# Optimization experiments

Hardware: AMD Instinct MI355X
Metric: run time of the kernel (lower is better)

Reference implementation:

```python
import jax, jax.numpy as jnp
import numpy as np

B, S, D_IN, D_H, D_ACT = 16, 2048, 1024, 2048, 1024


def setup_inputs() -> dict:
    key = jax.random.key(0)
    ks = jax.random.split(key, 8)
    s_in = 1.0 / np.sqrt(D_IN)
    s_h = 1.0 / np.sqrt(D_H)
    return {
        "x": jax.random.normal(ks[0], (B, S, D_IN), dtype=jnp.float32),
        "W_init": jax.random.uniform(ks[1], (D_H, D_IN), jnp.float32, -s_in, s_in),
        "b_init": jax.random.uniform(ks[2], (D_H,), jnp.float32, -s_in, s_in),
        "W_ih": jax.random.uniform(ks[3], (D_H, D_H), jnp.float32, -s_h, s_h),
        "b_ih": jax.random.uniform(ks[4], (D_H,), jnp.float32, -s_h, s_h),
        "b_hh": jax.random.uniform(ks[5], (D_H,), jnp.float32, -s_h, s_h),
        "W_final": jax.random.uniform(ks[6], (D_ACT, D_H), jnp.float32, -s_h, s_h),
        "b_final": jax.random.uniform(ks[7], (D_ACT,), jnp.float32, -s_h, s_h),
    }


def reference(x, W_init, b_init, W_ih, b_ih, b_hh, W_final, b_final):
    # initial linear + relu: [B,S,D_IN] -> [B,S,D_H]
    h = jax.nn.relu(jnp.einsum('bsi,hi->bsh', x, W_init) + b_init)
    # per-timestep RNN with hidden reset to zero each step: the W_hh term
    # vanishes, so each step is relu(W_ih @ h_t + b_ih + b_hh) -> one GEMM.
    out = jax.nn.relu(jnp.einsum('bsh,gh->bsg', h, W_ih) + b_ih + b_hh)
    # final linear: [B,S,D_H] -> [B,S,D_ACT]
    return jnp.einsum('bsh,ah->bsa', out, W_final) + b_final
```

## Files before the change

kernel.cpp:

```cpp
#include <hip/hip_runtime.h>
#include <hip/hip_bf16.h>
#include <stdint.h>
#include <stddef.h>

typedef __bf16 bf16;
typedef __bf16 bf16x8 __attribute__((ext_vector_type(8)));
typedef float f32x4 __attribute__((ext_vector_type(4)));
typedef __attribute__((address_space(1))) void gvoid;
typedef __attribute__((address_space(3))) void lvoid;

#define FENCE() asm volatile("" ::: "memory")
#define VMCNT(n) asm volatile("s_waitcnt vmcnt(" #n ")" ::: "memory")
#define BARS() do { FENCE(); __builtin_amdgcn_s_barrier(); FENCE(); } while (0)

__global__ __launch_bounds__(256)
void cvt_f32_bf16(const float* __restrict__ in, bf16* __restrict__ out, int n8)
{
    int i = blockIdx.x * 256 + threadIdx.x;
    if (i >= n8) return;
    const f32x4* p = (const f32x4*)in + (size_t)i * 2;
    f32x4 a = p[0], b = p[1];
    bf16x8 o;
    o[0] = (bf16)a[0]; o[1] = (bf16)a[1]; o[2] = (bf16)a[2]; o[3] = (bf16)a[3];
    o[4] = (bf16)b[0]; o[5] = (bf16)b[1]; o[6] = (bf16)b[2]; o[7] = (bf16)b[3];
    *((bf16x8*)out + i) = o;
}

#define RDA(buf, mh) \
    _Pragma("unroll") \
    for (int m_ = 0; m_ < 4; ++m_) { \
        af[m_][0] = *(const bf16x8*)(rdA0 + (buf) * 16384 + ((mh) + m_) * 1024); \
        af[m_][1] = *(const bf16x8*)(rdA1 + (buf) * 16384 + ((mh) + m_) * 1024); \
    }

#define RDB(buf, dst, nb) \
    _Pragma("unroll") \
    for (int n_ = 0; n_ < 2; ++n_) { \
        dst[n_][0] = *(const bf16x8*)(rdB0 + (buf) * 16384 + ((nb) + n_) * 1024); \
        dst[n_][1] = *(const bf16x8*)(rdB1 + (buf) * 16384 + ((nb) + n_) * 1024); \
    }

#define STAGE(gsrc, lreg, h, kt) do { \
        const bf16* g_ = (gsrc) + (size_t)((h) * 128) * K + (size_t)(kt) * 64; \
        bf16* l_ = (lreg) + (h) * 8192 + wave * 1024; \
        __builtin_amdgcn_global_load_lds((gvoid*)g_,           (lvoid*)l_,         16, 0, 0); \
        __builtin_amdgcn_global_load_lds((gvoid*)(g_ + rowK8), (lvoid*)(l_ + 512), 16, 0, 0); \
    } while (0)

#define QUAD(mh, nh, bb) \
    _Pragma("unroll") \
    for (int h_ = 0; h_ < 2; ++h_) \
        _Pragma("unroll") \
        for (int m_ = 0; m_ < 4; ++m_) \
            _Pragma("unroll") \
            for (int n_ = 0; n_ < 2; ++n_) \
                acc[(mh)+m_][(nh)+n_] = __builtin_amdgcn_mfma_f32_16x16x32_bf16( \
                    af[m_][h_], bb[n_][h_], acc[(mh)+m_][(nh)+n_], 0, 0, 0);

#define MFMA_PH(mh, nh, bb) do { \
        __builtin_amdgcn_s_setprio(1); QUAD(mh, nh, bb); __builtin_amdgcn_s_setprio(0); \
    } while (0)

template<int RELU, int TWO_BIAS, int OUTF32>
__global__ __launch_bounds__(512, 2)
void gemm256(const bf16* __restrict__ A, const bf16* __restrict__ Bm,
             const float* __restrict__ bias1, const float* __restrict__ bias2,
             void* __restrict__ Cp, int M, int N, int K)
{
    extern __shared__ bf16 smem[];
    bf16* As = smem;
    bf16* Bs = smem + 32768;

    const int tid  = threadIdx.x;
    const int wave = tid >> 6;
    const int lane = tid & 63;
    const int wr   = wave >> 2;
    const int wc   = wave & 3;

    const int nwg = gridDim.x * gridDim.y;
    int wg = blockIdx.y * gridDim.x + blockIdx.x;
    wg = (wg & 7) * (nwg >> 3) + (wg >> 3);
    const int bn = wg % gridDim.x;
    const int bm = wg / gridDim.x;

    const int rc  = lane >> 3;
    const int sgc = ((lane & 7) ^ rc) * 8;
    const bf16* aS0 = A  + (size_t)(bm * 256 + wave * 16 + rc) * K + sgc;
    const bf16* bS0 = Bm + (size_t)(bn * 256 + wave * 16 + rc) * K + sgc;
    const size_t rowK8 = (size_t)8 * K;

    const int frow = lane & 15;
    const int fg   = lane >> 4;
    const int fsw  = frow & 7;

    const bf16* rdA0 = As + wr * 8192 + frow * 64 + ((fg ^ fsw) << 3);
    const bf16* rdA1 = As + wr * 8192 + frow * 64 + (((fg + 4) ^ fsw) << 3);
    const bf16* rdB0 = Bs + (wc >> 1) * 8192 + (wc & 1) * 4096 + frow * 64 + ((fg ^ fsw) << 3);
    const bf16* rdB1 = Bs + (wc >> 1) * 8192 + (wc & 1) * 4096 + frow * 64 + (((fg + 4) ^ fsw) << 3);

    bf16x8 af[4][2], bl[2][2], bh[2][2];
    f32x4 acc[8][4];
    #pragma unroll
    for (int i = 0; i < 8; ++i)
        #pragma unroll
        for (int j = 0; j < 4; ++j)
            acc[i][j] = {0.f, 0.f, 0.f, 0.f};

    const int NT = K >> 6;
    const int NI = NT >> 1;

    STAGE(bS0, Bs,         0, 0); STAGE(bS0, Bs,         1, 0);
    STAGE(aS0, As,         0, 0); STAGE(aS0, As,         1, 0);
    STAGE(bS0, Bs + 16384, 0, 1); STAGE(bS0, Bs + 16384, 1, 1);
    VMCNT(4);
    BARS();

    for (int it = 0; it < NI; ++it) {
        const int t1 = 2 * it + 1;
        const int t2 = (2 * it + 2 < NT) ? 2 * it + 2 : 0;
        const int t3 = t2 + 1;

        RDB(0, bl, 0);
        RDA(0, 0);
        STAGE(aS0, As + 16384, 0, t1);
        BARS();
        MFMA_PH(0, 0, bl);
        RDB(0, bh, 2);
        STAGE(aS0, As + 16384, 1, t1);
        BARS();
        MFMA_PH(0, 2, bh);
        RDA(0, 4);
        BARS();
        MFMA_PH(4, 0, bl);
        STAGE(bS0, Bs, 0, t2);
        STAGE(bS0, Bs, 1, t2);
        VMCNT(4);
        BARS();
        MFMA_PH(4, 2, bh);
        RDB(1, bl, 0);
        RDA(1, 0);
        STAGE(aS0, As, 0, t2);
        BARS();
        MFMA_PH(0, 0, bl);
        RDB(1, bh, 2);
        STAGE(aS0, As, 1, t2);
        BARS();
        MFMA_PH(0, 2, bh);
        RDA(1, 4);
        BARS();
        MFMA_PH(4, 0, bl);
        STAGE(bS0, Bs + 16384, 0, t3);
        STAGE(bS0, Bs + 16384, 1, t3);
        VMCNT(4);
        BARS();
        MFMA_PH(4, 2, bh);
    }
    VMCNT(0);

    const int crow0 = bm * 256 + wr * 128 + (lane >> 4) * 4;
    const int ccol0 = bn * 256 + wc * 64 + (lane & 15);

    float bv[4];
    #pragma unroll
    for (int n = 0; n < 4; ++n) {
        bv[n] = bias1[ccol0 + n * 16];
        if (TWO_BIAS) bv[n] += bias2[ccol0 + n * 16];
    }

    #pragma unroll
    for (int m = 0; m < 8; ++m) {
        #pragma unroll
        for (int r = 0; r < 4; ++r) {
            const size_t row = (size_t)(crow0 + m * 16 + r);
            #pragma unroll
            for (int n = 0; n < 4; ++n) {
                float v = acc[m][n][r] + bv[n];
                if (RELU) v = fmaxf(v, 0.0f);
                if (OUTF32)
                    ((float*)Cp)[row * N + ccol0 + n * 16] = v;
                else
                    ((bf16*)Cp)[row * N + ccol0 + n * 16] = (bf16)v;
            }
        }
    }
}

static inline int cvt_blocks(size_t n) { return (int)((n / 8 + 255) / 256); }

extern "C" void kernel_launch(void* const* d_in, const int* in_sizes, int n_in,
                              void* d_out, int out_size, void* d_ws, size_t ws_size,
                              hipStream_t stream) {
    const float* x       = (const float*)d_in[0];
    const float* W_init  = (const float*)d_in[1];
    const float* b_init  = (const float*)d_in[2];
    const float* W_ih    = (const float*)d_in[3];
    const float* b_ih    = (const float*)d_in[4];
    const float* b_hh    = (const float*)d_in[5];
    const float* W_final = (const float*)d_in[6];
    const float* b_final = (const float*)d_in[7];
    float* out = (float*)d_out;

    const int D_H   = in_sizes[2];
    const int D_IN  = in_sizes[1] / D_H;
    const int D_ACT = in_sizes[7];
    const int M     = in_sizes[0] / D_IN;

    const size_t nx  = (size_t)M * D_IN;
    const size_t nw1 = (size_t)D_H * D_IN;
    const size_t nw2 = (size_t)D_H * D_H;
    const size_t nw3 = (size_t)D_ACT * D_H;
    const size_t nh  = (size_t)M * D_H;

    char* ws  = (char*)d_ws;
    bf16* h   = (bf16*)ws;
    bf16* a2  = (bf16*)(ws + nh * 2);
    bf16* xb  = a2;
    bf16* w1b = (bf16*)(ws + nh * 4);
    bf16* w2b = w1b + nw1;
    bf16* w3b = w2b + nw2;

    (void)hipFuncSetAttribute(reinterpret_cast<const void*>(&gemm256<1, 0, 0>),
                              hipFuncAttributeMaxDynamicSharedMemorySize, 131072);
    (void)hipFuncSetAttribute(reinterpret_cast<const void*>(&gemm256<1, 1, 0>),
                              hipFuncAttributeMaxDynamicSharedMemorySize, 131072);
    (void)hipFuncSetAttribute(reinterpret_cast<const void*>(&gemm256<0, 0, 1>),
                              hipFuncAttributeMaxDynamicSharedMemorySize, 131072);

    cvt_f32_bf16<<<cvt_blocks(nx),  256, 0, stream>>>(x,       xb,  (int)(nx  / 8));
    cvt_f32_bf16<<<cvt_blocks(nw1), 256, 0, stream>>>(W_init,  w1b, (int)(nw1 / 8));
    cvt_f32_bf16<<<cvt_blocks(nw2), 256, 0, stream>>>(W_ih,    w2b, (int)(nw2 / 8));
    cvt_f32_bf16<<<cvt_blocks(nw3), 256, 0, stream>>>(W_final, w3b, (int)(nw3 / 8));

    gemm256<1, 0, 0><<<dim3(D_H / 256, M / 256), 512, 131072, stream>>>(
        xb, w1b, b_init, nullptr, h, M, D_H, D_IN);

    gemm256<1, 1, 0><<<dim3(D_H / 256, M / 256), 512, 131072, stream>>>(
        h, w2b, b_ih, b_hh, a2, M, D_H, D_H);

    gemm256<0, 0, 1><<<dim3(D_ACT / 256, M / 256), 512, 131072, stream>>>(
        a2, w3b, b_final, nullptr, out, M, D_ACT, D_H);
}
```

Baseline: 699.8 us.

## Switch GEMM to 32x32x16 MFMA with restructured LDS read and prefetch schedule

Replaces the 16x16x32 bf16 MFMA tiling with 32x32x16 MFMA, so each wave holds 4x2 accumulators of 16 floats, and rewrites the LDS fragment addressing to match. The main loop is rescheduled into eight k-substeps with even/odd register double-buffering of fragments, and A and B tiles are staged together with full vmcnt(0) waits. The goal is fewer LDS reads per FLOP and denser MFMA issue. The cost is that the stricter vmcnt(0) waits may expose more global-load latency than the old partial waits did.

```diff
diff --git a/kernel.cpp b/kernel.cpp
--- a/kernel.cpp
+++ b/kernel.cpp
@@ -6,6 +6,7 @@
 typedef __bf16 bf16;
 typedef __bf16 bf16x8 __attribute__((ext_vector_type(8)));
 typedef float f32x4 __attribute__((ext_vector_type(4)));
+typedef float f32x16 __attribute__((ext_vector_type(16)));
 typedef __attribute__((address_space(1))) void gvoid;
 typedef __attribute__((address_space(3))) void lvoid;
 
@@ -26,19 +27,14 @@
     *((bf16x8*)out + i) = o;
 }
 
-#define RDA(buf, mh) \
-    _Pragma("unroll") \
-    for (int m_ = 0; m_ < 4; ++m_) { \
-        af[m_][0] = *(const bf16x8*)(rdA0 + (buf) * 16384 + ((mh) + m_) * 1024); \
-        af[m_][1] = *(const bf16x8*)(rdA1 + (buf) * 16384 + ((mh) + m_) * 1024); \
-    }
-
-#define RDB(buf, dst, nb) \
-    _Pragma("unroll") \
-    for (int n_ = 0; n_ < 2; ++n_) { \
-        dst[n_][0] = *(const bf16x8*)(rdB0 + (buf) * 16384 + ((nb) + n_) * 1024); \
-        dst[n_][1] = *(const bf16x8*)(rdB1 + (buf) * 16384 + ((nb) + n_) * 1024); \
-    }
+#define RD6(aset, bset, buf, ks) do { \
+        aset[0] = *(const bf16x8*)(aAddr[ks] + (buf) * 16384 + 0 * 2048); \
+        aset[1] = *(const bf16x8*)(aAddr[ks] + (buf) * 16384 + 1 * 2048); \
+        aset[2] = *(const bf16x8*)(aAddr[ks] + (buf) * 16384 + 2 * 2048); \
+        aset[3] = *(const bf16x8*)(aAddr[ks] + (buf) * 16384 + 3 * 2048); \
+        bset[0] = *(const bf16x8*)(bAddr[ks] + (buf) * 16384 + 0 * 2048); \
+        bset[1] = *(const bf16x8*)(bAddr[ks] + (buf) * 16384 + 1 * 2048); \
+    } while (0)
 
 #define STAGE(gsrc, lreg, h, kt) do { \
         const bf16* g_ = (gsrc) + (size_t)((h) * 128) * K + (size_t)(kt) * 64; \
@@ -47,18 +43,15 @@
         __builtin_amdgcn_global_load_lds((gvoid*)(g_ + rowK8), (lvoid*)(l_ + 512), 16, 0, 0); \
     } while (0)
 
-#define QUAD(mh, nh, bb) \
-    _Pragma("unroll") \
-    for (int h_ = 0; h_ < 2; ++h_) \
+#define MFMA8(aset, bset) do { \
+        __builtin_amdgcn_s_setprio(1); \
         _Pragma("unroll") \
-        for (int m_ = 0; m_ < 4; ++m_) \
+        for (int mb_ = 0; mb_ < 4; ++mb_) \
             _Pragma("unroll") \
-            for (int n_ = 0; n_ < 2; ++n_) \
-                acc[(mh)+m_][(nh)+n_] = __builtin_amdgcn_mfma_f32_16x16x32_bf16( \
-                    af[m_][h_], bb[n_][h_], acc[(mh)+m_][(nh)+n_], 0, 0, 0);
-
-#define MFMA_PH(mh, nh, bb) do { \
-        __builtin_amdgcn_s_setprio(1); QUAD(mh, nh, bb); __builtin_amdgcn_s_setprio(0); \
+            for (int nb_ = 0; nb_ < 2; ++nb_) \
+                acc[mb_][nb_] = __builtin_amdgcn_mfma_f32_32x32x16_bf16( \
+                    aset[mb_], bset[nb_], acc[mb_][nb_], 0, 0, 0); \
+        __builtin_amdgcn_s_setprio(0); \
     } while (0)
 
 template<int RELU, int TWO_BIAS, int OUTF32>
@@ -89,97 +82,103 @@
     const bf16* bS0 = Bm + (size_t)(bn * 256 + wave * 16 + rc) * K + sgc;
     const size_t rowK8 = (size_t)8 * K;
 
-    const int frow = lane & 15;
-    const int fg   = lane >> 4;
-    const int fsw  = frow & 7;
-
-    const bf16* rdA0 = As + wr * 8192 + frow * 64 + ((fg ^ fsw) << 3);
-    const bf16* rdA1 = As + wr * 8192 + frow * 64 + (((fg + 4) ^ fsw) << 3);
-    const bf16* rdB0 = Bs + (wc >> 1) * 8192 + (wc & 1) * 4096 + frow * 64 + ((fg ^ fsw) << 3);
-    const bf16* rdB1 = Bs + (wc >> 1) * 8192 + (wc & 1) * 4096 + frow * 64 + (((fg + 4) ^ fsw) << 3);
-
-    bf16x8 af[4][2], bl[2][2], bh[2][2];
-    f32x4 acc[8][4];
-    #pragma unroll
-    for (int i = 0; i < 8; ++i)
+    const int l31 = lane & 31;
+    const int lh  = lane >> 5;
+    const int fsw = lane & 7;
+
+    const bf16* aAddr[4];
+    const bf16* bAddr[4];
+    #pragma unroll
+    for (int ks = 0; ks < 4; ++ks) {
+        const int slot = (2 * ks + lh) ^ fsw;
+        aAddr[ks] = As + wr * 8192 + l31 * 64 + slot * 8;
+        bAddr[ks] = Bs + (wc >> 1) * 8192 + (wc & 1) * 4096 + l31 * 64 + slot * 8;
+    }
+
+    bf16x8 afE[4], afO[4], bbE[2], bbO[2];
+    f32x16 acc[4][2];
+    #pragma unroll
+    for (int i = 0; i < 4; ++i)
         #pragma unroll
-        for (int j = 0; j < 4; ++j)
-            acc[i][j] = {0.f, 0.f, 0.f, 0.f};
+        for (int j = 0; j < 2; ++j)
+            acc[i][j] = (f32x16)(0.f);
 
     const int NT = K >> 6;
     const int NI = NT >> 1;
 
-    STAGE(bS0, Bs,         0, 0); STAGE(bS0, Bs,         1, 0);
-    STAGE(aS0, As,         0, 0); STAGE(aS0, As,         1, 0);
-    STAGE(bS0, Bs + 16384, 0, 1); STAGE(bS0, Bs + 16384, 1, 1);
-    VMCNT(4);
+    STAGE(aS0, As, 0, 0); STAGE(aS0, As, 1, 0);
+    STAGE(bS0, Bs, 0, 0); STAGE(bS0, Bs, 1, 0);
+    VMCNT(0);
     BARS();
+    RD6(afE, bbE, 0, 0);
 
     for (int it = 0; it < NI; ++it) {
         const int t1 = 2 * it + 1;
         const int t2 = (2 * it + 2 < NT) ? 2 * it + 2 : 0;
-        const int t3 = t2 + 1;
-
-        RDB(0, bl, 0);
-        RDA(0, 0);
+
+        BARS();
+        MFMA8(afE, bbE);
+        RD6(afO, bbO, 0, 1);
         STAGE(aS0, As + 16384, 0, t1);
-        BARS();
-        MFMA_PH(0, 0, bl);
-        RDB(0, bh, 2);
         STAGE(aS0, As + 16384, 1, t1);
         BARS();
-        MFMA_PH(0, 2, bh);
-        RDA(0, 4);
-        BARS();
-        MFMA_PH(4, 0, bl);
+        MFMA8(afO, bbO);
+        RD6(afE, bbE, 0, 2);
+        STAGE(bS0, Bs + 16384, 0, t1);
+        STAGE(bS0, Bs + 16384, 1, t1);
+        BARS();
+        MFMA8(afE, bbE);
+        RD6(afO, bbO, 0, 3);
+        VMCNT(0);
+        BARS();
+        MFMA8(afO, bbO);
+        RD6(afE, bbE, 1, 0);
+        BARS();
+        MFMA8(afE, bbE);
+        RD6(afO, bbO, 1, 1);
+        STAGE(aS0, As, 0, t2);
+        STAGE(aS0, As, 1, t2);
+        BARS();
+        MFMA8(afO, bbO);
+        RD6(afE, bbE, 1, 2);
         STAGE(bS0, Bs, 0, t2);
         STAGE(bS0, Bs, 1, t2);
-        VMCNT(4);
-        BARS();
-        MFMA_PH(4, 2, bh);
-        RDB(1, bl, 0);
-        RDA(1, 0);
-        STAGE(aS0, As, 0, t2);
-        BARS();
-        MFMA_PH(0, 0, bl);
-        RDB(1, bh, 2);
-        STAGE(aS0, As, 1, t2);
-        BARS();
-        MFMA_PH(0, 2, bh);
-        RDA(1, 4);
-        BARS();
-        MFMA_PH(4, 0, bl);
-        STAGE(bS0, Bs + 16384, 0, t3);
-        STAGE(bS0, Bs + 16384, 1, t3);
-        VMCNT(4);
-        BARS();
-        MFMA_PH(4, 2, bh);
+        BARS();
+        MFMA8(afE, bbE);
+        RD6(afO, bbO, 1, 3);
+        VMCNT(0);
+        BARS();
+        MFMA8(afO, bbO);
+        RD6(afE, bbE, 0, 0);
     }
     VMCNT(0);
 
-    const int crow0 = bm * 256 + wr * 128 + (lane >> 4) * 4;
-    const int ccol0 = bn * 256 + wc * 64 + (lane & 15);
-
-    float bv[4];
-    #pragma unroll
-    for (int n = 0; n < 4; ++n) {
-        bv[n] = bias1[ccol0 + n * 16];
-        if (TWO_BIAS) bv[n] += bias2[ccol0 + n * 16];
-    }
-
-    #pragma unroll
-    for (int m = 0; m < 8; ++m) {
+    const int crow0 = bm * 256 + wr * 128 + 4 * lh;
+    const int ccol0 = bn * 256 + wc * 64 + l31;
+
+    float bv[2];
+    #pragma unroll
+    for (int nb = 0; nb < 2; ++nb) {
+        bv[nb] = bias1[ccol0 + nb * 32];
+        if (TWO_BIAS) bv[nb] += bias2[ccol0 + nb * 32];
+    }
+
+    #pragma unroll
+    for (int mb = 0; mb < 4; ++mb) {
         #pragma unroll
-        for (int r = 0; r < 4; ++r) {
-            const size_t row = (size_t)(crow0 + m * 16 + r);
+        for (int rq = 0; rq < 4; ++rq) {
             #pragma unroll
-            for (int n = 0; n < 4; ++n) {
-                float v = acc[m][n][r] + bv[n];
-                if (RELU) v = fmaxf(v, 0.0f);
-                if (OUTF32)
-                    ((float*)Cp)[row * N + ccol0 + n * 16] = v;
-                else
-                    ((bf16*)Cp)[row * N + ccol0 + n * 16] = (bf16)v;
+            for (int rl = 0; rl < 4; ++rl) {
+                const size_t row = (size_t)(crow0 + mb * 32 + rq * 8 + rl);
+                #pragma unroll
+                for (int nb = 0; nb < 2; ++nb) {
+                    float v = acc[mb][nb][rq * 4 + rl] + bv[nb];
+                    if (RELU) v = fmaxf(v, 0.0f);
+                    if (OUTF32)
+                        ((float*)Cp)[row * N + ccol0 + nb * 32] = v;
+                    else
+                        ((bf16*)Cp)[row * N + ccol0 + nb * 32] = (bf16)v;
+                }
             }
         }
     }
```

After: 772.9 us. 10.4% more time.
